# Kernel optimization log

Hardware: AMD Instinct MI355X
Metric: run time of the kernel (lower is better)

The kernel has to match this reference:

```python
import jax, jax.numpy as jnp
import numpy as np

B, TE, TD, H = 8, 512, 128, 256

def setup_inputs() -> dict:
    key = jax.random.key(0)
    k1, k2, k3, k4, k5 = jax.random.split(key, 5)
    return {
        "encoder_outputs": jax.random.normal(k1, (B, TE, H), dtype=jnp.float32),
        "decoder_outputs": jax.random.normal(k2, (B, TD, H), dtype=jnp.float32),
        "W_a": jax.random.normal(k3, (H, H), dtype=jnp.float32) * (1.0 / np.sqrt(H)),
        "U_a": jax.random.normal(k4, (H, H), dtype=jnp.float32) * (1.0 / np.sqrt(H)),
        "V_a": jax.random.normal(k5, (H, 1), dtype=jnp.float32) * (1.0 / np.sqrt(H)),
    }

def reference(encoder_outputs, decoder_outputs, W_a, U_a, V_a):
    # Bahdanau additive attention.
    enc_proj = jnp.einsum("beh,hk->bek", encoder_outputs, W_a)   # [B,TE,H]
    dec_proj = jnp.einsum("bdh,hk->bdk", decoder_outputs, U_a)   # [B,TD,H]
    # Broadcast add -> tanh -> project with V_a: [B,TD,TE]
    score = jnp.tanh(enc_proj[:, None, :, :] + dec_proj[:, :, None, :])  # [B,TD,TE,H]
    score = jnp.einsum("bdeh,h->bde", score, V_a[:, 0])          # [B,TD,TE]
    attention_weights = jax.nn.softmax(score, axis=-1)           # over encoder positions
    context = jnp.einsum("bde,beh->bdh", attention_weights, encoder_outputs)
    return (context, attention_weights)
```

## Files before the change

kernel.cpp:

```cpp
#include <hip/hip_runtime.h>
#include <hip/hip_bf16.h>

#ifndef __has_builtin
#define __has_builtin(x) 0
#endif

constexpr int B_ = 8, TE_ = 512, TD_ = 128, H_ = 256;
constexpr float TWO_LOG2E = 2.8853900817779268f;
constexpr float LOG2E = 1.4426950408889634f;

typedef float  vf2    __attribute__((ext_vector_type(2)));
typedef short  bf16x8 __attribute__((ext_vector_type(8)));
typedef float  f32x4  __attribute__((ext_vector_type(4)));

__device__ __forceinline__ float exp2_fast(float x) {
#if __has_builtin(__builtin_amdgcn_exp2f)
  return __builtin_amdgcn_exp2f(x);
#else
  return exp2f(x);
#endif
}
__device__ __forceinline__ float rcp_fast(float x) {
#if __has_builtin(__builtin_amdgcn_rcpf)
  return __builtin_amdgcn_rcpf(x);
#else
  return 1.0f / x;
#endif
}
__device__ __forceinline__ vf2 fma2(vf2 a, vf2 b, vf2 c) {
#if __has_builtin(__builtin_elementwise_fma)
  return __builtin_elementwise_fma(a, b, c);
#else
  vf2 r; r.x = __fmaf_rn(a.x, b.x, c.x); r.y = __fmaf_rn(a.y, b.y, c.y); return r;
#endif
}
__device__ __forceinline__ void bf16split(float x, unsigned short& hi, unsigned short& lo) {
  unsigned u = __float_as_uint(x);
  hi = (unsigned short)(u >> 16);
  float hif = __uint_as_float((unsigned)hi << 16);
  lo = (unsigned short)(__float_as_uint(x - hif) >> 16);
}

__global__ __launch_bounds__(256)
void proj_mfma(const float* __restrict__ enc, const float* __restrict__ dec,
               const float* __restrict__ W, const float* __restrict__ U,
               float* __restrict__ ep, float* __restrict__ dp) {
  __shared__ unsigned short Ah[32][40], Al[32][40], Bh[32][40], Bl[32][40];
  const int tid = threadIdx.x;
  const int mt = blockIdx.x;
  const int n0 = blockIdx.y * 32;
  const float* A; const float* Bm; float* C; int row0;
  if (mt < 128) { A = enc; Bm = W; C = ep; row0 = mt * 32; }
  else          { A = dec; Bm = U; C = dp; row0 = (mt - 128) * 32; }
  const int w = tid >> 6, lane = tid & 63;
  const int mw = (w & 1) * 16, nw = (w >> 1) * 16;
  const int quad = lane >> 4, l16 = lane & 15;
  const int am = tid >> 3, ak = (tid & 7) * 4;
  const int bn = tid & 31, bk = (tid >> 5) * 4;

  f32x4 acc = {0.f, 0.f, 0.f, 0.f};
  for (int k0 = 0; k0 < H_; k0 += 32) {
    float4 a4 = *(const float4*)&A[(long)(row0 + am) * H_ + k0 + ak];
    unsigned short h0, l0, h1, l1, h2, l2, h3, l3;
    bf16split(a4.x, h0, l0); bf16split(a4.y, h1, l1);
    bf16split(a4.z, h2, l2); bf16split(a4.w, h3, l3);
    *(ushort4*)&Ah[am][ak] = make_ushort4(h0, h1, h2, h3);
    *(ushort4*)&Al[am][ak] = make_ushort4(l0, l1, l2, l3);
    float b0 = Bm[(long)(k0 + bk + 0) * H_ + n0 + bn];
    float b1 = Bm[(long)(k0 + bk + 1) * H_ + n0 + bn];
    float b2 = Bm[(long)(k0 + bk + 2) * H_ + n0 + bn];
    float b3 = Bm[(long)(k0 + bk + 3) * H_ + n0 + bn];
    bf16split(b0, h0, l0); bf16split(b1, h1, l1);
    bf16split(b2, h2, l2); bf16split(b3, h3, l3);
    *(ushort4*)&Bh[bn][bk] = make_ushort4(h0, h1, h2, h3);
    *(ushort4*)&Bl[bn][bk] = make_ushort4(l0, l1, l2, l3);
    __syncthreads();
    bf16x8 ah = *(const bf16x8*)&Ah[mw + l16][quad * 8];
    bf16x8 al = *(const bf16x8*)&Al[mw + l16][quad * 8];
    bf16x8 bh = *(const bf16x8*)&Bh[nw + l16][quad * 8];
    bf16x8 bl = *(const bf16x8*)&Bl[nw + l16][quad * 8];
    acc = __builtin_amdgcn_mfma_f32_16x16x32_bf16(ah, bh, acc, 0, 0, 0);
    acc = __builtin_amdgcn_mfma_f32_16x16x32_bf16(ah, bl, acc, 0, 0, 0);
    acc = __builtin_amdgcn_mfma_f32_16x16x32_bf16(al, bh, acc, 0, 0, 0);
    __syncthreads();
  }
#pragma unroll
  for (int r = 0; r < 4; ++r)
    C[(long)(row0 + mw + quad * 4 + r) * H_ + n0 + nw + l16] = acc[r] * TWO_LOG2E;
}

__global__ __launch_bounds__(256)
void score_kernel(const float* __restrict__ ep, const float* __restrict__ dp,
                  const float* __restrict__ v, float* __restrict__ sc) {
  __shared__ __align__(16) float eps[32][68];
  __shared__ __align__(16) float dps[16][68];
  __shared__ __align__(16) float vs[64];
  const int tid = threadIdx.x;
  const int bz = blockIdx.z;
  const int b = bz >> 1;
  const int h_lo = (bz & 1) * 128;
  const int e0 = blockIdx.x * 32;
  const int d0 = blockIdx.y * 16;
  const int e = tid & 31;
  const int dg = tid >> 5;
  vf2 acc0 = {0.f, 0.f}, acc1 = {0.f, 0.f};

  for (int h0 = h_lo; h0 < h_lo + 128; h0 += 64) {
#pragma unroll
    for (int i = 0; i < 2; ++i) {
      int idx = tid + i * 256;
      int r = idx >> 4, c = (idx & 15) << 2;
      *(float4*)&eps[r][c] = *(const float4*)&ep[(long)(b * TE_ + e0 + r) * H_ + h0 + c];
    }
    {
      int r = tid >> 4, c = (tid & 15) << 2;
      *(float4*)&dps[r][c] = *(const float4*)&dp[(long)(b * TD_ + d0 + r) * H_ + h0 + c];
    }
    if (tid < 16) {
      float4 v4 = *(const float4*)&v[h0 + tid * 4];
      float4 o; o.x = -2.f * v4.x; o.y = -2.f * v4.y; o.z = -2.f * v4.z; o.w = -2.f * v4.w;
      *(float4*)&vs[tid * 4] = o;
    }
    __syncthreads();
    const vf2 one2 = {1.f, 1.f};
#pragma unroll
    for (int hh = 0; hh < 64; hh += 4) {
      float4 evf = *(const float4*)&eps[e][hh];
      float4 vvf = *(const float4*)&vs[hh];
      float4 daf = *(const float4*)&dps[dg * 2 + 0][hh];
      float4 dbf = *(const float4*)&dps[dg * 2 + 1][hh];
      vf2 ev0 = {evf.x, evf.y}, ev1 = {evf.z, evf.w};
      vf2 vv0 = {vvf.x, vvf.y}, vv1 = {vvf.z, vvf.w};
      vf2 da0 = {daf.x, daf.y}, da1 = {daf.z, daf.w};
      vf2 db0 = {dbf.x, dbf.y}, db1 = {dbf.z, dbf.w};
      vf2 g0 = ev0 + da0, g1 = ev1 + da1;
      vf2 h0v = ev0 + db0, h1v = ev1 + db1;
      vf2 t0, t1, u0, u1;
      t0.x = exp2_fast(g0.x); t0.y = exp2_fast(g0.y);
      t1.x = exp2_fast(g1.x); t1.y = exp2_fast(g1.y);
      u0.x = exp2_fast(h0v.x); u0.y = exp2_fast(h0v.y);
      u1.x = exp2_fast(h1v.x); u1.y = exp2_fast(h1v.y);
      t0 = t0 + one2; t1 = t1 + one2; u0 = u0 + one2; u1 = u1 + one2;
      vf2 r0, r1, s0, s1;
      r0.x = rcp_fast(t0.x); r0.y = rcp_fast(t0.y);
      r1.x = rcp_fast(t1.x); r1.y = rcp_fast(t1.y);
      s0.x = rcp_fast(u0.x); s0.y = rcp_fast(u0.y);
      s1.x = rcp_fast(u1.x); s1.y = rcp_fast(u1.y);
      acc0 = fma2(vv0, r0, acc0); acc0 = fma2(vv1, r1, acc0);
      acc1 = fma2(vv0, s0, acc1); acc1 = fma2(vv1, s1, acc1);
    }
    __syncthreads();
  }
  long base = ((long)(bz & 1) * B_ * TD_ + (long)b * TD_ + d0 + dg * 2) * TE_ + e0 + e;
  sc[base] = acc0.x + acc0.y;
  sc[base + TE_] = acc1.x + acc1.y;
}

__global__ __launch_bounds__(64)
void softmax_kernel(const float* __restrict__ sc, float* __restrict__ attn) {
  const long row = blockIdx.x;
  const float* p0 = sc + row * TE_;
  const float* p1 = sc + ((long)B_ * TD_ + row) * TE_;
  float* pout = attn + row * TE_;
  const int t = threadIdx.x;
  float x[8];
  float m = -1e30f;
#pragma unroll
  for (int k = 0; k < 8; ++k) {
    x[k] = p0[t + 64 * k] + p1[t + 64 * k];
    m = fmaxf(m, x[k]);
  }
#pragma unroll
  for (int off = 32; off; off >>= 1) m = fmaxf(m, __shfl_xor(m, off, 64));
  float s = 0.f;
#pragma unroll
  for (int k = 0; k < 8; ++k) { x[k] = exp2_fast((x[k] - m) * LOG2E); s += x[k]; }
#pragma unroll
  for (int off = 32; off; off >>= 1) s += __shfl_xor(s, off, 64);
  const float r = rcp_fast(s);
#pragma unroll
  for (int k = 0; k < 8; ++k) pout[t + 64 * k] = x[k] * r;
}

__global__ __launch_bounds__(256)
void ctx_mfma(const float* __restrict__ attn, const float* __restrict__ enc,
              float* __restrict__ ctx) {
  __shared__ unsigned short Ah[32][40], Al[32][40], Bh[32][40], Bl[32][40];
  const int tid = threadIdx.x;
  const int m0 = blockIdx.x * 32;
  const int n0 = blockIdx.y * 32;
  const int b = blockIdx.z;
  const float* A = attn + (long)b * TD_ * TE_;
  const float* E = enc + (long)b * TE_ * H_;
  const int w = tid >> 6, lane = tid & 63;
  const int mw = (w & 1) * 16, nw = (w >> 1) * 16;
  const int quad = lane >> 4, l16 = lane & 15;
  const int am = tid >> 3, ak = (tid & 7) * 4;
  const int bn = tid & 31, bk = (tid >> 5) * 4;

  f32x4 acc = {0.f, 0.f, 0.f, 0.f};
  for (int k0 = 0; k0 < TE_; k0 += 32) {
    float4 a4 = *(const float4*)&A[(long)(m0 + am) * TE_ + k0 + ak];
    unsigned short h0, l0, h1, l1, h2, l2, h3, l3;
    bf16split(a4.x, h0, l0); bf16split(a4.y, h1, l1);
    bf16split(a4.z, h2, l2); bf16split(a4.w, h3, l3);
    *(ushort4*)&Ah[am][ak] = make_ushort4(h0, h1, h2, h3);
    *(ushort4*)&Al[am][ak] = make_ushort4(l0, l1, l2, l3);
    float b0 = E[(long)(k0 + bk + 0) * H_ + n0 + bn];
    float b1 = E[(long)(k0 + bk + 1) * H_ + n0 + bn];
    float b2 = E[(long)(k0 + bk + 2) * H_ + n0 + bn];
    float b3 = E[(long)(k0 + bk + 3) * H_ + n0 + bn];
    bf16split(b0, h0, l0); bf16split(b1, h1, l1);
    bf16split(b2, h2, l2); bf16split(b3, h3, l3);
    *(ushort4*)&Bh[bn][bk] = make_ushort4(h0, h1, h2, h3);
    *(ushort4*)&Bl[bn][bk] = make_ushort4(l0, l1, l2, l3);
    __syncthreads();
    bf16x8 ah = *(const bf16x8*)&Ah[mw + l16][quad * 8];
    bf16x8 al = *(const bf16x8*)&Al[mw + l16][quad * 8];
    bf16x8 bh = *(const bf16x8*)&Bh[nw + l16][quad * 8];
    bf16x8 bl = *(const bf16x8*)&Bl[nw + l16][quad * 8];
    acc = __builtin_amdgcn_mfma_f32_16x16x32_bf16(ah, bh, acc, 0, 0, 0);
    acc = __builtin_amdgcn_mfma_f32_16x16x32_bf16(ah, bl, acc, 0, 0, 0);
    acc = __builtin_amdgcn_mfma_f32_16x16x32_bf16(al, bh, acc, 0, 0, 0);
    __syncthreads();
  }
#pragma unroll
  for (int r = 0; r < 4; ++r)
    ctx[((long)b * TD_ + m0 + mw + quad * 4 + r) * H_ + n0 + nw + l16] = acc[r];
}

extern "C" void kernel_launch(void* const* d_in, const int* in_sizes, int n_in,
                              void* d_out, int out_size, void* d_ws, size_t ws_size,
                              hipStream_t stream) {
  const float* enc = (const float*)d_in[0];
  const float* dec = (const float*)d_in[1];
  const float* Wa  = (const float*)d_in[2];
  const float* Ua  = (const float*)d_in[3];
  const float* Va  = (const float*)d_in[4];

  float* out  = (float*)d_out;
  float* ctx  = out;
  float* attn = out + (long)B_ * TD_ * H_;

  float* ep = (float*)d_ws;
  float* dp = ep + (long)B_ * TE_ * H_;
  float* sc = dp + (long)B_ * TD_ * H_;

  proj_mfma<<<dim3(160, 8), 256, 0, stream>>>(enc, dec, Wa, Ua, ep, dp);
  score_kernel<<<dim3(TE_ / 32, TD_ / 16, 2 * B_), 256, 0, stream>>>(ep, dp, Va, sc);
  softmax_kernel<<<dim3(B_ * TD_), 64, 0, stream>>>(sc, attn);
  ctx_mfma<<<dim3(TD_ / 32, H_ / 32, B_), 256, 0, stream>>>(attn, enc, ctx);
}
```

Baseline: 109.1 us.

## Fuse softmax into context GEMM, recomputing row statistics per block

Drops the separate softmax kernel. Each context-GEMM block now computes the row max and log-sum for its 32 rows from the two partial score buffers, then rebuilds the probabilities on the fly while loading its A tile. Only blocks with n0==0 write the attention weights. This saves one kernel launch and the write-then-read of the attention matrix, at the cost of every one of the 8 column blocks redoing the row statistics and exponentials.

Measured after the change: 115.9 us. +6.3%, slower.

```diff
diff --git a/kernel.cpp b/kernel.cpp
--- a/kernel.cpp
+++ b/kernel.cpp
@@ -156,72 +156,80 @@
   sc[base + TE_] = acc1.x + acc1.y;
 }
 
-__global__ __launch_bounds__(64)
-void softmax_kernel(const float* __restrict__ sc, float* __restrict__ attn) {
-  const long row = blockIdx.x;
-  const float* p0 = sc + row * TE_;
-  const float* p1 = sc + ((long)B_ * TD_ + row) * TE_;
-  float* pout = attn + row * TE_;
-  const int t = threadIdx.x;
-  float x[8];
-  float m = -1e30f;
-#pragma unroll
-  for (int k = 0; k < 8; ++k) {
-    x[k] = p0[t + 64 * k] + p1[t + 64 * k];
-    m = fmaxf(m, x[k]);
-  }
-#pragma unroll
-  for (int off = 32; off; off >>= 1) m = fmaxf(m, __shfl_xor(m, off, 64));
-  float s = 0.f;
-#pragma unroll
-  for (int k = 0; k < 8; ++k) { x[k] = exp2_fast((x[k] - m) * LOG2E); s += x[k]; }
-#pragma unroll
-  for (int off = 32; off; off >>= 1) s += __shfl_xor(s, off, 64);
-  const float r = rcp_fast(s);
-#pragma unroll
-  for (int k = 0; k < 8; ++k) pout[t + 64 * k] = x[k] * r;
-}
-
 __global__ __launch_bounds__(256)
-void ctx_mfma(const float* __restrict__ attn, const float* __restrict__ enc,
-              float* __restrict__ ctx) {
-  __shared__ unsigned short Ah[32][40], Al[32][40], Bh[32][40], Bl[32][40];
+void ctx_sm(const float* __restrict__ sc, const float* __restrict__ enc,
+            float* __restrict__ attn, float* __restrict__ ctx) {
+  __shared__ unsigned short Ph[32][40], Pl[32][40], Eh[32][40], El[32][40];
+  __shared__ float rowc[32];
   const int tid = threadIdx.x;
   const int m0 = blockIdx.x * 32;
   const int n0 = blockIdx.y * 32;
-  const int b = blockIdx.z;
-  const float* A = attn + (long)b * TD_ * TE_;
-  const float* E = enc + (long)b * TE_ * H_;
+  const int b  = blockIdx.z;
   const int w = tid >> 6, lane = tid & 63;
+  const float* s0 = sc + ((long)b * TD_ + m0) * TE_;
+  const float* s1 = sc + ((long)B_ * TD_ + (long)b * TD_ + m0) * TE_;
+
+  for (int rr = 0; rr < 8; ++rr) {
+    const int r = w * 8 + rr;
+    const float* p0 = s0 + (long)r * TE_;
+    const float* p1 = s1 + (long)r * TE_;
+    float x[8]; float mx = -1e30f;
+#pragma unroll
+    for (int k = 0; k < 8; ++k) {
+      x[k] = p0[lane + 64 * k] + p1[lane + 64 * k];
+      mx = fmaxf(mx, x[k]);
+    }
+#pragma unroll
+    for (int off = 32; off; off >>= 1) mx = fmaxf(mx, __shfl_xor(mx, off, 64));
+    float sum = 0.f;
+#pragma unroll
+    for (int k = 0; k < 8; ++k) sum += exp2_fast((x[k] - mx) * LOG2E);
+#pragma unroll
+    for (int off = 32; off; off >>= 1) sum += __shfl_xor(sum, off, 64);
+    if (lane == 0) rowc[r] = -(mx * LOG2E) - __log2f(sum);
+  }
+  __syncthreads();
+
   const int mw = (w & 1) * 16, nw = (w >> 1) * 16;
   const int quad = lane >> 4, l16 = lane & 15;
   const int am = tid >> 3, ak = (tid & 7) * 4;
   const int bn = tid & 31, bk = (tid >> 5) * 4;
+  const float c0 = rowc[am];
+  const float* E = enc + (long)b * TE_ * H_;
+  const bool writeAttn = (n0 == 0);
+  float* arow = attn + ((long)b * TD_ + m0 + am) * TE_;
 
   f32x4 acc = {0.f, 0.f, 0.f, 0.f};
   for (int k0 = 0; k0 < TE_; k0 += 32) {
-    float4 a4 = *(const float4*)&A[(long)(m0 + am) * TE_ + k0 + ak];
+    float4 a0 = *(const float4*)&s0[(long)am * TE_ + k0 + ak];
+    float4 a1 = *(const float4*)&s1[(long)am * TE_ + k0 + ak];
+    float4 p;
+    p.x = exp2_fast(__fmaf_rn(a0.x + a1.x, LOG2E, c0));
+    p.y = exp2_fast(__fmaf_rn(a0.y + a1.y, LOG2E, c0));
+    p.z = exp2_fast(__fmaf_rn(a0.z + a1.z, LOG2E, c0));
+    p.w = exp2_fast(__fmaf_rn(a0.w + a1.w, LOG2E, c0));
     unsigned short h0, l0, h1, l1, h2, l2, h3, l3;
-    bf16split(a4.x, h0, l0); bf16split(a4.y, h1, l1);
-    bf16split(a4.z, h2, l2); bf16split(a4.w, h3, l3);
-    *(ushort4*)&Ah[am][ak] = make_ushort4(h0, h1, h2, h3);
-    *(ushort4*)&Al[am][ak] = make_ushort4(l0, l1, l2, l3);
+    bf16split(p.x, h0, l0); bf16split(p.y, h1, l1);
+    bf16split(p.z, h2, l2); bf16split(p.w, h3, l3);
+    *(ushort4*)&Ph[am][ak] = make_ushort4(h0, h1, h2, h3);
+    *(ushort4*)&Pl[am][ak] = make_ushort4(l0, l1, l2, l3);
+    if (writeAttn) *(float4*)&arow[k0 + ak] = p;
     float b0 = E[(long)(k0 + bk + 0) * H_ + n0 + bn];
     float b1 = E[(long)(k0 + bk + 1) * H_ + n0 + bn];
     float b2 = E[(long)(k0 + bk + 2) * H_ + n0 + bn];
     float b3 = E[(long)(k0 + bk + 3) * H_ + n0 + bn];
     bf16split(b0, h0, l0); bf16split(b1, h1, l1);
     bf16split(b2, h2, l2); bf16split(b3, h3, l3);
-    *(ushort4*)&Bh[bn][bk] = make_ushort4(h0, h1, h2, h3);
-    *(ushort4*)&Bl[bn][bk] = make_ushort4(l0, l1, l2, l3);
-    __syncthreads();
-    bf16x8 ah = *(const bf16x8*)&Ah[mw + l16][quad * 8];
-    bf16x8 al = *(const bf16x8*)&Al[mw + l16][quad * 8];
-    bf16x8 bh = *(const bf16x8*)&Bh[nw + l16][quad * 8];
-    bf16x8 bl = *(const bf16x8*)&Bl[nw + l16][quad * 8];
-    acc = __builtin_amdgcn_mfma_f32_16x16x32_bf16(ah, bh, acc, 0, 0, 0);
-    acc = __builtin_amdgcn_mfma_f32_16x16x32_bf16(ah, bl, acc, 0, 0, 0);
-    acc = __builtin_amdgcn_mfma_f32_16x16x32_bf16(al, bh, acc, 0, 0, 0);
+    *(ushort4*)&Eh[bn][bk] = make_ushort4(h0, h1, h2, h3);
+    *(ushort4*)&El[bn][bk] = make_ushort4(l0, l1, l2, l3);
+    __syncthreads();
+    bf16x8 ph = *(const bf16x8*)&Ph[mw + l16][quad * 8];
+    bf16x8 pl = *(const bf16x8*)&Pl[mw + l16][quad * 8];
+    bf16x8 eh = *(const bf16x8*)&Eh[nw + l16][quad * 8];
+    bf16x8 el = *(const bf16x8*)&El[nw + l16][quad * 8];
+    acc = __builtin_amdgcn_mfma_f32_16x16x32_bf16(ph, eh, acc, 0, 0, 0);
+    acc = __builtin_amdgcn_mfma_f32_16x16x32_bf16(ph, el, acc, 0, 0, 0);
+    acc = __builtin_amdgcn_mfma_f32_16x16x32_bf16(pl, eh, acc, 0, 0, 0);
     __syncthreads();
   }
 #pragma unroll
@@ -248,6 +256,5 @@
 
   proj_mfma<<<dim3(160, 8), 256, 0, stream>>>(enc, dec, Wa, Ua, ep, dp);
   score_kernel<<<dim3(TE_ / 32, TD_ / 16, 2 * B_), 256, 0, stream>>>(ep, dp, Va, sc);
-  softmax_kernel<<<dim3(B_ * TD_), 64, 0, stream>>>(sc, attn);
-  ctx_mfma<<<dim3(TD_ / 32, H_ / 32, B_), 256, 0, stream>>>(attn, enc, ctx);
-}
+  ctx_sm<<<dim3(TD_ / 32, H_ / 32, B_), 256, 0, stream>>>(sc, enc, attn, ctx);
+}
```
